# Kernel tuning notes

Measured on AMD Instinct MI355X. Metric: run time of the kernel, lower is better.

Reference implementation:

```python
import jax, jax.numpy as jnp
import numpy as np
from jax import lax

N_STM = 65536
N_LTM = 65536
TOP_M = 2048        # consolidation_top_m
KAPPA = 0.05        # consolidation_kappa
XI_H = 0.005
XI_E = 0.003
RHO_F = 0.2         # normalization_rho_f
C_V = 2.0           # normalization_c_v
SIGMA = 2.0         # blur_sigma
THRESH = 0.5        # new_center_threshold
EPS = 1e-8


def _gauss_kernel(sigma, radius=6):
    x = jnp.arange(-radius, radius + 1, dtype=jnp.float32)
    k = jnp.exp(-0.5 * (x / sigma) ** 2)
    return k / jnp.sum(k)


def _blur1d(x, k, axis):
    # depthwise gaussian 1D conv along `axis` of x [C,D,H,W]
    xm = jnp.moveaxis(x, axis, -1)
    shp = xm.shape
    inp = xm.reshape(-1, 1, shp[-1])                       # [B,1,L]
    out = lax.conv_general_dilated(inp, k[None, None, :], (1,), 'SAME')
    return jnp.moveaxis(out.reshape(shp), -1, axis)


def _blur3d(x, sigma):
    k = _gauss_kernel(sigma)
    for ax in (1, 2, 3):
        x = _blur1d(x, k, ax)
    return x


def setup_inputs() -> dict:
    key = jax.random.key(0)
    ks = jax.random.split(key, 16)
    return {
        'stm_K': jax.random.normal(ks[0], (N_STM, 16), jnp.float32),
        'stm_V': jax.random.normal(ks[1], (N_STM, 128), jnp.float32),
        'stm_e': jax.random.normal(ks[2], (N_STM, 4), jnp.float32),
        'stm_h': jax.random.uniform(ks[3], (N_STM,), jnp.float32),
        'ltm_K': jax.random.normal(ks[4], (N_LTM, 64), jnp.float32),
        'ltm_V': jax.random.normal(ks[5], (N_LTM, 128), jnp.float32),
        'ltm_e': jax.random.normal(ks[6], (N_LTM, 4), jnp.float32),
        'ltm_h': jax.random.uniform(ks[7], (N_LTM,), jnp.float32),
        'W_proj': jax.random.normal(ks[8], (16, 64), jnp.float32) * 0.25,
        'b_proj': jax.random.normal(ks[9], (64,), jnp.float32) * 0.02,
        'stm_terrain': jax.random.normal(ks[10], (5, 96, 96, 96), jnp.float32),
        'ltm_terrain': jax.random.normal(ks[11], (5, 96, 96, 96), jnp.float32),
        'fatigue': jnp.float32(12.0),
        'stm_active': jax.random.randint(ks[12], (N_STM,), 0, 2, jnp.int32),
        'ltm_active': jax.random.randint(ks[13], (N_LTM,), 0, 2, jnp.int32),
    }


def reference(stm_K, stm_V, stm_e, stm_h, ltm_K, ltm_V, ltm_e, ltm_h,
              W_proj, b_proj, stm_terrain, ltm_terrain, fatigue,
              stm_active, ltm_active):
    N = ltm_K.shape[0]
    # --- select top-M active STM centers by intensity h ---
    h_masked = jnp.where(stm_active > 0, stm_h, -jnp.inf)
    _, sel = lax.top_k(h_masked, TOP_M)                    # [M]
    K_sel = stm_K[sel]                                     # [M, d_stm]
    V_sel = stm_V[sel]                                     # [M, d_v]
    e_sel = stm_e[sel]                                     # [M, d_e]
    omega = KAPPA * stm_h[sel]                             # [M] write intensity
    # --- project STM keys into LTM key space ---
    K_proj = K_sel @ W_proj + b_proj                       # [M, d_ltm]
    # --- match against existing active LTM centers (cosine sim) ---
    ltm_act = ltm_active > 0
    kp = K_proj / (jnp.linalg.norm(K_proj, axis=-1, keepdims=True) + EPS)
    lk = ltm_K / (jnp.linalg.norm(ltm_K, axis=-1, keepdims=True) + EPS)
    sims = kp @ lk.T                                       # [M, N] (dominant traffic)
    sims = jnp.where(ltm_act[None, :], sims, -jnp.inf)
    best = jnp.argmax(sims, axis=1)                        # [M]
    best_sim = jnp.max(sims, axis=1)                       # [M]
    matched = best_sim >= THRESH
    # --- matched: intensity-weighted additive write into best center ---
    idx_m = jnp.where(matched, best, N)                    # N -> dropped (OOB)
    ltm_K2 = ltm_K.at[idx_m].add(omega[:, None] * K_proj, mode='drop')
    ltm_V2 = ltm_V.at[idx_m].add(omega[:, None] * V_sel, mode='drop')
    ltm_e2 = ltm_e.at[idx_m].add(omega[:, None] * e_sel, mode='drop')
    ltm_h2 = ltm_h.at[idx_m].add(omega, mode='drop')
    # --- unmatched: allocate fresh inactive slots (stable: inactive first) ---
    unmatched = ~matched
    rank = jnp.cumsum(unmatched.astype(jnp.int32)) - 1
    free_slots = jnp.argsort(ltm_act.astype(jnp.int32))    # inactive indices first
    slot = free_slots[jnp.clip(rank, 0, N - 1)]
    idx_n = jnp.where(unmatched, slot, N)
    ltm_K2 = ltm_K2.at[idx_n].set(K_proj, mode='drop')
    ltm_V2 = ltm_V2.at[idx_n].set(V_sel, mode='drop')
    ltm_e2 = ltm_e2.at[idx_n].set(e_sel, mode='drop')
    ltm_h2 = ltm_h2.at[idx_n].set(omega, mode='drop')
    # --- terrain merge: ltm += xi * gaussian_blur(stm), h vs emotion rates ---
    blurred = _blur3d(stm_terrain, SIGMA)
    xi = jnp.array([XI_H, XI_E, XI_E, XI_E, XI_E], jnp.float32).reshape(5, 1, 1, 1)
    ltm_terrain2 = ltm_terrain + xi * blurred
    # --- STM value normalization: clip row norms to c_v ---
    vnorm = jnp.linalg.norm(stm_V, axis=-1, keepdims=True)
    stm_V2 = stm_V * jnp.minimum(1.0, C_V / (vnorm + EPS))
    # --- fatigue decay ---
    fatigue2 = RHO_F * fatigue
    return (ltm_K2, ltm_V2, ltm_e2, ltm_h2, stm_V2, ltm_terrain2, fatigue2)
```

## Files before the change

kernel.cpp:

```cpp
#include <hip/hip_runtime.h>
#include <hip/hip_bf16.h>
#include <cfloat>
#include <cstdint>

#define N_STM 65536
#define N_LTM 65536
#define TOPM 2048
#define NBINS 4096
#define CAND_CAP 4096
#define NSPL 512
#define WCAP 8192
#define KAPPA 0.05f
#define EPS_F 1e-8f
#define THRESH 0.5f
#define MARGIN 0.01f

typedef __attribute__((ext_vector_type(8))) __bf16 bf16x8;
typedef __attribute__((ext_vector_type(4))) float f32x4;

__device__ __forceinline__ unsigned int f2ord(float f) {
  unsigned int b = __float_as_uint(f);
  return b ^ ((b & 0x80000000u) ? 0xFFFFFFFFu : 0x80000000u);
}
__device__ __forceinline__ float ord2f(unsigned int u) {
  unsigned int b = (u & 0x80000000u) ? (u ^ 0x80000000u) : ~u;
  return __uint_as_float(b);
}
__device__ __forceinline__ unsigned short f2bf(float f) {
  __hip_bfloat16 h = __float2bfloat16(f);
  return __builtin_bit_cast(unsigned short, h);
}
__device__ __forceinline__ unsigned long long shflxor64(unsigned long long v, int mask) {
  unsigned int lo = (unsigned int)v, hi = (unsigned int)(v >> 32);
  lo = __shfl_xor(lo, mask, 64);
  hi = __shfl_xor(hi, mask, 64);
  return ((unsigned long long)hi << 32) | lo;
}

__global__ void k_zero(int* __restrict__ hist, int* __restrict__ counts,
                       int* __restrict__ candcnt, int* __restrict__ wcnt,
                       unsigned long long* __restrict__ finalkey) {
  int i = blockIdx.x * 256 + threadIdx.x;
  hist[i] = 0;
  if (i < 2048) finalkey[i] = 0ull;
  if (i < 256) counts[i] = 0;
  if (i == 0) { candcnt[0] = 0; wcnt[0] = 0; }
}

__global__ void k_hist(const float* __restrict__ h, const int* __restrict__ act,
                       int* __restrict__ hist) {
  int i = blockIdx.x * blockDim.x + threadIdx.x;
  if (i >= N_STM) return;
  if (act[i] > 0) {
    float v = h[i];
    int b = (int)(v * (float)NBINS);
    b = min(max(b, 0), NBINS - 1);
    atomicAdd(&hist[b], 1);
  }
}

__global__ __launch_bounds__(1024) void k_thresh(const int* __restrict__ hist,
                                                 int* __restrict__ thrbin) {
  __shared__ int t[1024];
  int tid = threadIdx.x;
  int c0 = hist[tid * 4 + 0], c1 = hist[tid * 4 + 1];
  int c2 = hist[tid * 4 + 2], c3 = hist[tid * 4 + 3];
  int local = c0 + c1 + c2 + c3;
  t[tid] = local;
  __syncthreads();
  for (int off = 1; off < 1024; off <<= 1) {
    int v = (tid + off < 1024) ? t[tid + off] : 0;
    __syncthreads();
    t[tid] += v;
    __syncthreads();
  }
  int after = t[tid] - local;
  int s3 = c3, s2 = c2 + s3, s1 = c1 + s2, s0 = c0 + s1;
  int S0 = after + s0, S1 = after + s1, S2 = after + s2, S3 = after + s3, S4 = after;
  if (S0 >= TOPM && S1 < TOPM) *thrbin = tid * 4 + 0;
  if (S1 >= TOPM && S2 < TOPM) *thrbin = tid * 4 + 1;
  if (S2 >= TOPM && S3 < TOPM) *thrbin = tid * 4 + 2;
  if (S3 >= TOPM && S4 < TOPM) *thrbin = tid * 4 + 3;
}

__global__ void k_gather(const float* __restrict__ h, const int* __restrict__ act,
                         const int* __restrict__ thrbin,
                         unsigned long long* __restrict__ cand, int* __restrict__ cnt) {
  int i = blockIdx.x * blockDim.x + threadIdx.x;
  if (i >= N_STM) return;
  if (act[i] > 0) {
    float v = h[i];
    int b = (int)(v * (float)NBINS);
    b = min(max(b, 0), NBINS - 1);
    if (b >= *thrbin) {
      int pos = atomicAdd(cnt, 1);
      if (pos < CAND_CAP)
        cand[pos] = ((unsigned long long)f2ord(v) << 32) |
                    (unsigned long long)(0xFFFFFFFFu - (unsigned)i);
    }
  }
}

__global__ __launch_bounds__(1024) void k_sortsel(const float* __restrict__ h,
                                                  const unsigned long long* __restrict__ cand,
                                                  const int* __restrict__ cnt,
                                                  int* __restrict__ sel,
                                                  float* __restrict__ omega) {
  __shared__ unsigned long long d[CAND_CAP];
  int tid = threadIdx.x;
  int n = *cnt; if (n > CAND_CAP) n = CAND_CAP;
  for (int i = tid; i < CAND_CAP; i += 1024) d[i] = (i < n) ? cand[i] : 0ull;
  __syncthreads();
  for (int k = 2; k <= CAND_CAP; k <<= 1) {
    for (int j = k >> 1; j > 0; j >>= 1) {
      for (int i = tid; i < CAND_CAP; i += 1024) {
        int ixj = i ^ j;
        if (ixj > i) {
          unsigned long long a = d[i], b = d[ixj];
          bool up = ((i & k) == 0);
          bool sw = up ? (a < b) : (a > b);
          if (sw) { d[i] = b; d[ixj] = a; }
        }
      }
      __syncthreads();
    }
  }
  for (int i = tid; i < TOPM; i += 1024) {
    unsigned int inv = (unsigned int)(d[i] & 0xFFFFFFFFull);
    int idx = (int)(0xFFFFFFFFu - inv);
    sel[i] = idx;
    omega[i] = KAPPA * h[idx];
  }
}

__global__ void k_lknorm(const float* __restrict__ lk, const int* __restrict__ act,
                         float* __restrict__ lkn, unsigned short* __restrict__ lknb) {
  int tid = threadIdx.x;
  int row = blockIdx.x * 4 + (tid >> 6);
  int lane = tid & 63;
  float v = lk[row * 64 + lane];
  float ss = v * v;
  for (int off = 32; off; off >>= 1) ss += __shfl_xor(ss, off, 64);
  float denom = sqrtf(ss) + EPS_F;
  float r = (act[row] > 0) ? (v / denom) : 0.0f;
  lkn[row * 64 + lane] = r;
  lknb[row * 64 + lane] = f2bf(r);
}

__global__ void k_proj(const float* __restrict__ stmK, const float* __restrict__ W,
                       const float* __restrict__ bp, const int* __restrict__ sel,
                       float* __restrict__ Kproj, float* __restrict__ kpn,
                       unsigned short* __restrict__ kpnb) {
  int m = blockIdx.x;
  int j = threadIdx.x;
  int s = sel[m];
  float acc = bp[j];
#pragma unroll
  for (int k = 0; k < 16; ++k) acc += stmK[s * 16 + k] * W[k * 64 + j];
  float ss = acc * acc;
  for (int off = 32; off; off >>= 1) ss += __shfl_xor(ss, off, 64);
  float denom = sqrtf(ss) + EPS_F;
  float r = acc / denom;
  Kproj[m * 64 + j] = acc;
  kpn[m * 64 + j] = r;
  kpnb[m * 64 + j] = f2bf(r);
}

__global__ __launch_bounds__(512) void k_simmax(const unsigned short* __restrict__ kpnb,
                                                const unsigned short* __restrict__ lknb,
                                                float* __restrict__ partials) {
  __shared__ char lds[16384];
  int tid = threadIdx.x;
  int lane = tid & 63, w = tid >> 6;
  int lg = lane >> 4, lc = lane & 15;
  int nbase = blockIdx.x * 128;
  int mbase = blockIdx.y * 256;

#pragma unroll
  for (int r = 0; r < 2; ++r) {
    int slot = r * 512 + tid;
    int kh = (slot >> 6) & 1;
    int t  = slot >> 7;
    const unsigned short* src = lknb + (size_t)(nbase + t * 16 + lc) * 64 + kh * 32 + lg * 8;
    char* dst = &lds[(size_t)(r * 512 + w * 64) * 16];
    __builtin_amdgcn_global_load_lds((const __attribute__((address_space(1))) void*)src,
                                     (__attribute__((address_space(3))) void*)dst, 16, 0, 0);
  }

  bf16x8 a[2][2];
#pragma unroll
  for (int g = 0; g < 2; ++g)
#pragma unroll
    for (int kh = 0; kh < 2; ++kh)
      a[g][kh] = *reinterpret_cast<const bf16x8*>(
          kpnb + (size_t)(mbase + w * 32 + g * 16 + lc) * 64 + kh * 32 + lg * 8);

  float bmax[2][4];
#pragma unroll
  for (int g = 0; g < 2; ++g)
#pragma unroll
    for (int r = 0; r < 4; ++r) bmax[g][r] = -FLT_MAX;

  __syncthreads();

#pragma unroll
  for (int t = 0; t < 8; ++t) {
    bf16x8 b0 = *reinterpret_cast<const bf16x8*>(&lds[(size_t)((t * 2 + 0) * 64 + lane) * 16]);
    bf16x8 b1 = *reinterpret_cast<const bf16x8*>(&lds[(size_t)((t * 2 + 1) * 64 + lane) * 16]);
#pragma unroll
    for (int g = 0; g < 2; ++g) {
      f32x4 z = {0.f, 0.f, 0.f, 0.f};
      f32x4 c = __builtin_amdgcn_mfma_f32_16x16x32_bf16(a[g][0], b0, z, 0, 0, 0);
      c = __builtin_amdgcn_mfma_f32_16x16x32_bf16(a[g][1], b1, c, 0, 0, 0);
#pragma unroll
      for (int r = 0; r < 4; ++r) bmax[g][r] = fmaxf(bmax[g][r], c[r]);
    }
  }

#pragma unroll
  for (int g = 0; g < 2; ++g)
#pragma unroll
    for (int r = 0; r < 4; ++r) {
      float v = bmax[g][r];
#pragma unroll
      for (int mk = 1; mk <= 8; mk <<= 1) v = fmaxf(v, __shfl_xor(v, mk, 64));
      bmax[g][r] = v;
    }
  if (lc == 0) {
#pragma unroll
    for (int g = 0; g < 2; ++g)
#pragma unroll
      for (int r = 0; r < 4; ++r)
        partials[(size_t)(mbase + w * 32 + g * 16 + lg * 4 + r) * NSPL + blockIdx.x] = bmax[g][r];
  }
}

__global__ __launch_bounds__(128) void k_redmax(const float* __restrict__ partials,
                                                int* __restrict__ worklist,
                                                int* __restrict__ wcnt) {
  int m = blockIdx.x;
  int tid = threadIdx.x;
  f32x4 v = ((const f32x4*)(partials + (size_t)m * NSPL))[tid];
  float mx = fmaxf(fmaxf(v[0], v[1]), fmaxf(v[2], v[3]));
  for (int mk = 1; mk <= 32; mk <<= 1) mx = fmaxf(mx, __shfl_xor(mx, mk, 64));
  __shared__ float s[2];
  if ((tid & 63) == 0) s[tid >> 6] = mx;
  __syncthreads();
  float thr = fmaxf(s[0], s[1]) - MARGIN;
#pragma unroll
  for (int q = 0; q < 4; ++q) {
    if (v[q] >= thr) {
      int pos = atomicAdd(wcnt, 1);
      if (pos < WCAP) worklist[pos] = m * NSPL + tid * 4 + q;
    }
  }
}

__global__ __launch_bounds__(64) void k_exact(const int* __restrict__ worklist,
                                              const int* __restrict__ wcnt,
                                              const float* __restrict__ kpn,
                                              const float* __restrict__ lkn,
                                              unsigned long long* __restrict__ finalkey) {
  int b = blockIdx.x;
  int cnt = *wcnt; if (cnt > WCAP) cnt = WCAP;
  if (b >= cnt) return;
  int e = worklist[b];
  int m = e >> 9, sp = e & (NSPL - 1);
  int lane = threadIdx.x;
  const float* ka = kpn + (size_t)m * 64;
  unsigned long long key = 0;
#pragma unroll
  for (int c = 0; c < 2; ++c) {
    int col = sp * 128 + c * 64 + lane;
    const float* kb = lkn + (size_t)col * 64;
    float ex = 0.f;
    for (int k = 0; k < 64; ++k) ex += ka[k] * kb[k];
    unsigned long long kk = ((unsigned long long)f2ord(ex) << 32) |
                            (unsigned long long)(0xFFFFFFFFu - (unsigned)col);
    if (kk > key) key = kk;
  }
  for (int mk = 1; mk <= 32; mk <<= 1) {
    unsigned long long o = shflxor64(key, mk);
    if (o > key) key = o;
  }
  if (lane == 0) atomicMax(finalkey + m, key);
}

__global__ void k_rank(const unsigned long long* __restrict__ finalkey,
                       int* __restrict__ best, int* __restrict__ matched,
                       int* __restrict__ rank,
                       const float* __restrict__ fatigue, float* __restrict__ outF) {
  __shared__ int s[256];
  int tid = threadIdx.x;
  int base = tid * 8;
  int flags[8]; int c = 0;
#pragma unroll
  for (int q = 0; q < 8; ++q) {
    unsigned long long k = finalkey[base + q];
    float v = ord2f((unsigned int)(k >> 32));
    int mt = (v >= THRESH) ? 1 : 0;
    matched[base + q] = mt;
    best[base + q] = (int)(0xFFFFFFFFu - (unsigned int)(k & 0xFFFFFFFFull));
    flags[q] = mt ? 0 : 1;
    c += flags[q];
  }
  s[tid] = c;
  __syncthreads();
  for (int off = 1; off < 256; off <<= 1) {
    int v = (tid >= off) ? s[tid - off] : 0;
    __syncthreads();
    s[tid] += v;
    __syncthreads();
  }
  int run = s[tid] - c;
#pragma unroll
  for (int q = 0; q < 8; ++q) {
    rank[base + q] = flags[q] ? run : -1;
    run += flags[q];
  }
  if (tid == 0) outF[0] = 0.2f * fatigue[0];
}

__global__ void k_cnt(const int* __restrict__ act, int* __restrict__ counts) {
  int i = blockIdx.x * 256 + threadIdx.x;
  int v = (act[i] == 0) ? 1 : 0;
  unsigned long long ball = __ballot(v);
  if ((threadIdx.x & 63) == 0) atomicAdd(&counts[blockIdx.x], __popcll(ball));
}

__global__ void k_scan256(const int* __restrict__ in, int* __restrict__ out) {
  __shared__ int s[256];
  int tid = threadIdx.x;
  int x = in[tid];
  s[tid] = x;
  __syncthreads();
  for (int off = 1; off < 256; off <<= 1) {
    int v = (tid >= off) ? s[tid - off] : 0;
    __syncthreads();
    s[tid] += v;
    __syncthreads();
  }
  out[tid] = s[tid] - x;
}

__global__ void k_compact(const int* __restrict__ act, const int* __restrict__ offsets,
                          int* __restrict__ inact) {
  __shared__ int s[256];
  int tid = threadIdx.x;
  int i = blockIdx.x * 256 + tid;
  int v = (act[i] == 0) ? 1 : 0;
  s[tid] = v;
  __syncthreads();
  for (int off = 1; off < 256; off <<= 1) {
    int u = (tid >= off) ? s[tid - off] : 0;
    __syncthreads();
    s[tid] += u;
    __syncthreads();
  }
  if (v) inact[offsets[blockIdx.x] + s[tid] - v] = i;
}

__global__ void k_scatter(const int* __restrict__ matched, const int* __restrict__ best,
                          const int* __restrict__ rank, const int* __restrict__ sel,
                          const float* __restrict__ omega, const float* __restrict__ Kproj,
                          const float* __restrict__ stmV, const float* __restrict__ stmE,
                          const int* __restrict__ inact,
                          float* __restrict__ outK, float* __restrict__ outV,
                          float* __restrict__ outE, float* __restrict__ outH) {
  int m = blockIdx.x;
  int t = threadIdx.x;
  int s = sel[m];
  float om = omega[m];
  if (matched[m]) {
    int b = best[m];
    if (t < 64) atomicAdd(&outK[b * 64 + t], om * Kproj[m * 64 + t]);
    atomicAdd(&outV[b * 128 + t], om * stmV[s * 128 + t]);
    if (t < 4) atomicAdd(&outE[b * 4 + t], om * stmE[s * 4 + t]);
    if (t == 0) atomicAdd(&outH[b], om);
  } else {
    int slot = inact[rank[m]];
    if (t < 64) outK[slot * 64 + t] = Kproj[m * 64 + t];
    outV[slot * 128 + t] = stmV[s * 128 + t];
    if (t < 4) outE[slot * 4 + t] = stmE[s * 4 + t];
    if (t == 0) outH[slot] = om;
  }
}

__global__ void k_vnorm(const float* __restrict__ V, float* __restrict__ out) {
  int tid = threadIdx.x;
  int row = blockIdx.x * 4 + (tid >> 6);
  int lane = tid & 63;
  float a = V[row * 128 + lane];
  float b = V[row * 128 + 64 + lane];
  float ss = a * a + b * b;
  for (int off = 32; off; off >>= 1) ss += __shfl_xor(ss, off, 64);
  float scale = fminf(1.0f, 2.0f / (sqrtf(ss) + EPS_F));
  out[row * 128 + lane] = a * scale;
  out[row * 128 + 64 + lane] = b * scale;
}

struct GW13 { float w[13]; };

__global__ void k_blurW(const float* __restrict__ in, float* __restrict__ out, GW13 g) {
  int idx = blockIdx.x * 256 + threadIdx.x;
  int w = idx % 96;
  float s = 0.f;
#pragma unroll
  for (int t = -6; t <= 6; ++t) {
    int ww = w + t;
    if (ww >= 0 && ww < 96) s += g.w[t + 6] * in[idx + t];
  }
  out[idx] = s;
}

__global__ void k_blurH(const float* __restrict__ in, float* __restrict__ out, GW13 g) {
  int idx = blockIdx.x * 256 + threadIdx.x;
  int h = (idx / 96) % 96;
  float s = 0.f;
#pragma unroll
  for (int t = -6; t <= 6; ++t) {
    int hh = h + t;
    if (hh >= 0 && hh < 96) s += g.w[t + 6] * in[idx + t * 96];
  }
  out[idx] = s;
}

__global__ void k_blurD(const float* __restrict__ in, const float* __restrict__ ltmT,
                        float* __restrict__ out, GW13 g) {
  int idx = blockIdx.x * 256 + threadIdx.x;
  int d = (idx / 9216) % 96;
  int c = idx / 884736;
  float s = 0.f;
#pragma unroll
  for (int t = -6; t <= 6; ++t) {
    int dd = d + t;
    if (dd >= 0 && dd < 96) s += g.w[t + 6] * in[idx + t * 9216];
  }
  float xi = (c == 0) ? 0.005f : 0.003f;
  out[idx] = ltmT[idx] + xi * s;
}

extern "C" void kernel_launch(void* const* d_in, const int* in_sizes, int n_in,
                              void* d_out, int out_size, void* d_ws, size_t ws_size,
                              hipStream_t stream) {
  const float* stmK = (const float*)d_in[0];
  const float* stmV = (const float*)d_in[1];
  const float* stmE = (const float*)d_in[2];
  const float* stmH = (const float*)d_in[3];
  const float* ltmK = (const float*)d_in[4];
  const float* ltmV = (const float*)d_in[5];
  const float* ltmE = (const float*)d_in[6];
  const float* ltmH = (const float*)d_in[7];
  const float* Wp   = (const float*)d_in[8];
  const float* bp   = (const float*)d_in[9];
  const float* sT   = (const float*)d_in[10];
  const float* lT   = (const float*)d_in[11];
  const float* fat  = (const float*)d_in[12];
  const int*   sAct = (const int*)d_in[13];
  const int*   lAct = (const int*)d_in[14];

  float* out = (float*)d_out;
  float* outK  = out;
  float* outV  = out + 4194304;
  float* outE  = out + 12582912;
  float* outH  = out + 12845056;
  float* outSV = out + 12910592;
  float* outT  = out + 21299200;
  float* outF  = out + 25722880;

  char* p = (char*)d_ws;
  auto alloc = [&](size_t bytes) -> void* {
    void* r = (void*)p;
    p += (bytes + 255) & ~(size_t)255;
    return r;
  };
  float* lkn      = (float*)alloc((size_t)N_LTM * 64 * 4);
  unsigned short* lknb = (unsigned short*)alloc((size_t)N_LTM * 64 * 2);
  float* kpn      = (float*)alloc((size_t)TOPM * 64 * 4);
  unsigned short* kpnb = (unsigned short*)alloc((size_t)TOPM * 64 * 2);
  float* Kproj    = (float*)alloc((size_t)TOPM * 64 * 4);
  unsigned long long* finalkey = (unsigned long long*)alloc(TOPM * 8);
  int*   wcnt     = (int*)alloc(256);
  int*   best     = (int*)alloc(TOPM * 4);
  int*   matched  = (int*)alloc(TOPM * 4);
  int*   rank     = (int*)alloc(TOPM * 4);
  int*   sel      = (int*)alloc(TOPM * 4);
  float* omega    = (float*)alloc(TOPM * 4);
  int*   hist     = (int*)alloc(NBINS * 4);
  int*   candcnt  = (int*)alloc(256);
  unsigned long long* cand = (unsigned long long*)alloc(CAND_CAP * 8);
  int*   thrbin   = (int*)alloc(256);
  int*   counts   = (int*)alloc(256 * 4);
  int*   offsets  = (int*)alloc(256 * 4);
  int*   inact    = (int*)alloc((size_t)N_LTM * 4);
  float* tmpA     = (float*)alloc((size_t)4423680 * 4);
  float* tmpB     = (float*)alloc((size_t)4423680 * 4);
  float* partials = tmpA;
  int* worklist = (int*)tmpB;
  (void)ws_size; (void)in_sizes; (void)n_in; (void)out_size;

  hipMemcpyAsync(outK, ltmK, (size_t)4194304 * 4, hipMemcpyDeviceToDevice, stream);
  hipMemcpyAsync(outV, ltmV, (size_t)8388608 * 4, hipMemcpyDeviceToDevice, stream);
  hipMemcpyAsync(outE, ltmE, (size_t)262144 * 4, hipMemcpyDeviceToDevice, stream);
  hipMemcpyAsync(outH, ltmH, (size_t)65536 * 4, hipMemcpyDeviceToDevice, stream);

  k_zero<<<16, 256, 0, stream>>>(hist, counts, candcnt, wcnt, finalkey);

  k_hist<<<256, 256, 0, stream>>>(stmH, sAct, hist);
  k_thresh<<<1, 1024, 0, stream>>>(hist, thrbin);
  k_gather<<<256, 256, 0, stream>>>(stmH, sAct, thrbin, cand, candcnt);
  k_sortsel<<<1, 1024, 0, stream>>>(stmH, cand, candcnt, sel, omega);

  k_lknorm<<<N_LTM / 4, 256, 0, stream>>>(ltmK, lAct, lkn, lknb);
  k_proj<<<TOPM, 64, 0, stream>>>(stmK, Wp, bp, sel, Kproj, kpn, kpnb);

  k_simmax<<<dim3(NSPL, 8), 512, 0, stream>>>(kpnb, lknb, partials);
  k_redmax<<<TOPM, 128, 0, stream>>>(partials, worklist, wcnt);
  k_exact<<<WCAP, 64, 0, stream>>>(worklist, wcnt, kpn, lkn, finalkey);

  k_rank<<<1, 256, 0, stream>>>(finalkey, best, matched, rank, fat, outF);
  k_cnt<<<256, 256, 0, stream>>>(lAct, counts);
  k_scan256<<<1, 256, 0, stream>>>(counts, offsets);
  k_compact<<<256, 256, 0, stream>>>(lAct, offsets, inact);

  k_scatter<<<TOPM, 128, 0, stream>>>(matched, best, rank, sel, omega, Kproj,
                                      stmV, stmE, inact, outK, outV, outE, outH);

  k_vnorm<<<N_STM / 4, 256, 0, stream>>>(stmV, outSV);

  GW13 g;
  {
    float s = 0.f;
    for (int i = -6; i <= 6; ++i) {
      float v = expf(-0.5f * ((float)i / 2.0f) * ((float)i / 2.0f));
      g.w[i + 6] = v;
      s += v;
    }
    for (int i = 0; i < 13; ++i) g.w[i] /= s;
  }
  int tblocks = 4423680 / 256;
  k_blurW<<<tblocks, 256, 0, stream>>>(sT, tmpA, g);
  k_blurH<<<tblocks, 256, 0, stream>>>(tmpA, tmpB, g);
  k_blurD<<<tblocks, 256, 0, stream>>>(tmpB, lT, outT, g);
}
```

Before: 542.5 us.

## Replace single-block bitonic sort with multi-block rank-by-counting selection

```diff
diff --git a/kernel.cpp b/kernel.cpp
--- a/kernel.cpp
+++ b/kernel.cpp
@@ -101,35 +101,27 @@
   }
 }
 
-__global__ __launch_bounds__(1024) void k_sortsel(const float* __restrict__ h,
-                                                  const unsigned long long* __restrict__ cand,
-                                                  const int* __restrict__ cnt,
-                                                  int* __restrict__ sel,
-                                                  float* __restrict__ omega) {
-  __shared__ unsigned long long d[CAND_CAP];
-  int tid = threadIdx.x;
-  int n = *cnt; if (n > CAND_CAP) n = CAND_CAP;
-  for (int i = tid; i < CAND_CAP; i += 1024) d[i] = (i < n) ? cand[i] : 0ull;
-  __syncthreads();
-  for (int k = 2; k <= CAND_CAP; k <<= 1) {
-    for (int j = k >> 1; j > 0; j >>= 1) {
-      for (int i = tid; i < CAND_CAP; i += 1024) {
-        int ixj = i ^ j;
-        if (ixj > i) {
-          unsigned long long a = d[i], b = d[ixj];
-          bool up = ((i & k) == 0);
-          bool sw = up ? (a < b) : (a > b);
-          if (sw) { d[i] = b; d[ixj] = a; }
-        }
-      }
-      __syncthreads();
-    }
-  }
-  for (int i = tid; i < TOPM; i += 1024) {
-    unsigned int inv = (unsigned int)(d[i] & 0xFFFFFFFFull);
-    int idx = (int)(0xFFFFFFFFu - inv);
-    sel[i] = idx;
-    omega[i] = KAPPA * h[idx];
+__global__ __launch_bounds__(256) void k_ranksel(const float* __restrict__ h,
+                                                 const unsigned long long* __restrict__ cand,
+                                                 const int* __restrict__ cnt,
+                                                 int* __restrict__ sel,
+                                                 float* __restrict__ omega) {
+  __shared__ unsigned long long keys[1024];
+  int C = *cnt; if (C > CAND_CAP) C = CAND_CAP;
+  int t = blockIdx.x * 256 + threadIdx.x;
+  unsigned long long mine = (t < C) ? cand[t] : 0ull;
+  int r = 0;
+  for (int base = 0; base < C; base += 1024) {
+    int lim = min(1024, C - base);
+    __syncthreads();
+    for (int j = threadIdx.x; j < lim; j += 256) keys[j] = cand[base + j];
+    __syncthreads();
+    for (int j = 0; j < lim; ++j) r += (keys[j] > mine) ? 1 : 0;
+  }
+  if (t < C && r < TOPM) {
+    int idx = (int)(0xFFFFFFFFu - (unsigned int)(mine & 0xFFFFFFFFull));
+    sel[r] = idx;
+    omega[r] = KAPPA * h[idx];
   }
 }
 
@@ -509,7 +501,7 @@
   k_hist<<<256, 256, 0, stream>>>(stmH, sAct, hist);
   k_thresh<<<1, 1024, 0, stream>>>(hist, thrbin);
   k_gather<<<256, 256, 0, stream>>>(stmH, sAct, thrbin, cand, candcnt);
-  k_sortsel<<<1, 1024, 0, stream>>>(stmH, cand, candcnt, sel, omega);
+  k_ranksel<<<16, 256, 0, stream>>>(stmH, cand, candcnt, sel, omega);
 
   k_lknorm<<<N_LTM / 4, 256, 0, stream>>>(ltmK, lAct, lkn, lknb);
   k_proj<<<TOPM, 64, 0, stream>>>(stmK, Wp, bp, sel, Kproj, kpn, kpnb);
```

Result: faster. 509.2 us (-6.2%).
